# Kernel tuning notes

Hardware: AMD Instinct MI355X
Metric: run time of the kernel (lower is better)

## Reference

```python
import jax, jax.numpy as jnp
from jax import lax
import numpy as np

# ---- constants mirroring args ----
T = 8192          # signal length
NUM_CH = 64       # eeg channels
LSTM_SIZE = 256
NUM_CLS = 40
NUM_PROP = 1024   # candidate proposals before NMS
NUM_PROP_AFTER = 256
PROP_LEN = 128    # extracted window length
IOU_THRESH = 0.5


def setup_inputs() -> dict:
    key = jax.random.key(0)
    ks = jax.random.split(key, 12)
    data = jax.random.normal(ks[0], (T, NUM_CH), dtype=jnp.float32)
    # proposals: (start, end, score), 1-D temporal intervals
    starts = jax.random.uniform(ks[1], (NUM_PROP,), minval=0.0, maxval=float(T - PROP_LEN))
    lens = jax.random.uniform(ks[2], (NUM_PROP,), minval=32.0, maxval=float(PROP_LEN))
    scores = jax.random.uniform(ks[3], (NUM_PROP,))
    proposals = jnp.stack([starts, starts + lens, scores], axis=-1).astype(jnp.float32)

    H, C = LSTM_SIZE, NUM_CH
    s_ih = 1.0 / np.sqrt(C)
    s_hh = 1.0 / np.sqrt(H)
    W_ih = jax.random.uniform(ks[4], (4 * H, C), minval=-s_ih, maxval=s_ih)
    W_hh = jax.random.uniform(ks[5], (4 * H, H), minval=-s_hh, maxval=s_hh)
    b_ih = jax.random.uniform(ks[6], (4 * H,), minval=-s_hh, maxval=s_hh)
    b_hh = jax.random.uniform(ks[7], (4 * H,), minval=-s_hh, maxval=s_hh)
    s_h = 1.0 / np.sqrt(H)
    W_cls = jax.random.uniform(ks[8], (NUM_CLS, H), minval=-s_h, maxval=s_h)
    b_cls = jax.random.uniform(ks[9], (NUM_CLS,), minval=-s_h, maxval=s_h)
    W_bbox = jax.random.uniform(ks[10], (2 * NUM_CLS, H), minval=-s_h, maxval=s_h)
    b_bbox = jax.random.uniform(ks[11], (2 * NUM_CLS,), minval=-s_h, maxval=s_h)
    return {"data": data, "proposals": proposals, "W_ih": W_ih, "W_hh": W_hh,
            "b_ih": b_ih, "b_hh": b_hh, "W_cls": W_cls, "b_cls": b_cls,
            "W_bbox": W_bbox, "b_bbox": b_bbox}


def _nms_1d(starts, ends, scores, iou_thresh):
    """Greedy 1-D interval NMS. Returns indices (into original order) of the
    first NUM_PROP_AFTER surviving proposals, in descending-score order."""
    order = jnp.argsort(-scores)
    s, e = starts[order], ends[order]
    n = s.shape[0]
    idx = jnp.arange(n)

    def body(i, sup):
        inter = jnp.maximum(0.0, jnp.minimum(e[i], e) - jnp.maximum(s[i], s))
        union = (e[i] - s[i]) + (e - s) - inter
        iou = inter / jnp.maximum(union, 1e-6)
        new = sup | ((iou > iou_thresh) & (idx > i) & (~sup[i]))
        return new

    suppressed = lax.fori_loop(0, n, body, jnp.zeros(n, dtype=bool))
    keep = ~suppressed
    # stable sort: kept proposals first, preserving score order
    sel = jnp.argsort(jnp.where(keep, 0, 1), stable=True)[:NUM_PROP_AFTER]
    return order[sel]


def _lstm_last(x, W_ih, W_hh, b_ih, b_hh):
    """x: [K, L, C]; returns last hidden state [K, H] (torch gate order ifgo)."""
    K = x.shape[0]
    H = W_hh.shape[1]
    h0 = jnp.zeros((K, H), x.dtype)
    c0 = jnp.zeros((K, H), x.dtype)
    b = b_ih + b_hh

    def step(carry, xt):
        h, c = carry
        gates = xt @ W_ih.T + h @ W_hh.T + b  # [K, 4H]
        i, f, g, o = jnp.split(gates, 4, axis=-1)
        i = jax.nn.sigmoid(i)
        f = jax.nn.sigmoid(f)
        g = jnp.tanh(g)
        o = jax.nn.sigmoid(o)
        c = f * c + i * g
        h = o * jnp.tanh(c)
        return (h, c), None

    (h, _), _ = lax.scan(step, (h0, c0), jnp.swapaxes(x, 0, 1))
    return h


def reference(data, proposals, W_ih, W_hh, b_ih, b_hh, W_cls, b_cls, W_bbox, b_bbox):
    starts, ends, scores = proposals[:, 0], proposals[:, 1], proposals[:, 2]
    # NMS + truncate to num_prop_after (training branch of original)
    kept = _nms_1d(starts, ends, scores, IOU_THRESH)            # [K]
    # extract fixed-length eeg windows at proposal starts (gather)
    t0 = jnp.clip(jnp.round(starts[kept]).astype(jnp.int32), 0, T - PROP_LEN)
    win_idx = t0[:, None] + jnp.arange(PROP_LEN)[None, :]       # [K, L]
    eeg_proposals = data[win_idx]                               # [K, L, C]
    # region LSTM -> last timestep feature
    base_feat = _lstm_last(eeg_proposals, W_ih, W_hh, b_ih, b_hh)  # [K, H]
    cls_feat = base_feat @ W_cls.T + b_cls                      # [K, num_cls]
    bbox_feat = base_feat @ W_bbox.T + b_bbox                   # [K, 2*num_cls]
    return cls_feat, bbox_feat
```

## Files before the change

### kernel.cpp

```cpp
#include <hip/hip_runtime.h>
#include <math.h>

#define T_LEN 8192
#define NUM_CH 64
#define HID 256
#define NUM_CLS 40
#define NUM_PROP 1024
#define NUM_PROP_AFTER 256
#define PROP_LEN 128

#define MS 4
#define NGRP 64
#define NSL 4
#define KH 320
#define KSEGN 4
#define SEGH 80

typedef _Float16 h2_t __attribute__((ext_vector_type(2)));
union U32H2 { unsigned int u; h2_t h; };
union HU16 { _Float16 h; unsigned short u; };

#if defined(__has_builtin)
#if __has_builtin(__builtin_amdgcn_fdot2)
#define HAS_FDOT2 1
#endif
#endif

__device__ __forceinline__ float dot2f(unsigned int wa, unsigned int hb, float acc) {
    U32H2 a, b;
    a.u = wa;
    b.u = hb;
#ifdef HAS_FDOT2
    return __builtin_amdgcn_fdot2(a.h, b.h, acc, false);
#else
    return acc + (float)a.h[0] * (float)b.h[0] + (float)a.h[1] * (float)b.h[1];
#endif
}

__device__ __forceinline__ float dot8f(const uint4& w, const uint4& h, float acc) {
    acc = dot2f(w.x, h.x, acc);
    acc = dot2f(w.y, h.y, acc);
    acc = dot2f(w.z, h.z, acc);
    acc = dot2f(w.w, h.w, acc);
    return acc;
}

__device__ __forceinline__ float fsigmoid(float x) { return 1.0f / (1.0f + __expf(-x)); }
__device__ __forceinline__ float ftanh(float x) {
    float e = __expf(-2.0f * fabsf(x));
    float t = (1.0f - e) / (1.0f + e);
    return copysignf(t, x);
}

__device__ __forceinline__ unsigned int pack2(float a, float b) {
    HU16 ha, hb;
    ha.h = (_Float16)a;
    hb.h = (_Float16)b;
    return (unsigned int)ha.u | ((unsigned int)hb.u << 16);
}

__global__ __launch_bounds__(1024, 4) void fused_kernel(
    const float* __restrict__ data, const float* __restrict__ prop,
    const float* __restrict__ W_ih, const float* __restrict__ W_hh,
    const float* __restrict__ b_ih, const float* __restrict__ b_hh,
    const float* __restrict__ W_cls, const float* __restrict__ b_cls,
    const float* __restrict__ W_bbox, const float* __restrict__ b_bbox,
    float* __restrict__ out, int* __restrict__ t0s,
    unsigned int* __restrict__ Hx, unsigned int* __restrict__ cnt,
    unsigned int* __restrict__ flag) {
    __shared__ __align__(16) _Float16 hx[MS][KH];
    __shared__ __align__(16) float pp[MS][KSEGN][256];

    const int tid = threadIdx.x;
    const int g = blockIdx.x & (NGRP - 1);
    const int s = blockIdx.x >> 6;
    const int kseg = tid >> 8;
    const int rl = tid & 255;

    if (blockIdx.x == 0) {
        float* sc_p = &pp[0][0][0];
        float* ss = &pp[1][0][0];
        float* se = &pp[2][0][0];
        unsigned char* sup = (unsigned char*)&pp[3][0][0];
        unsigned long long* cmask =
            (unsigned long long*)((char*)&pp[3][0][0] + 1024);

        float ps = prop[tid * 3 + 0];
        float pe = prop[tid * 3 + 1];
        float pc = prop[tid * 3 + 2];
        sc_p[tid] = pc;
        sup[tid] = 0;
        __syncthreads();

        int r = 0;
        for (int j = 0; j < NUM_PROP; ++j) {
            float o = sc_p[j];
            r += (o > pc) || (o == pc && j < tid);
        }
        ss[r] = ps;
        se[r] = pe;
        __syncthreads();

        const float my_s = ss[tid];
        const float my_e = se[tid];
        const float my_len = my_e - my_s;
        bool mysup = false;

        for (int ci = 0; ci < 16; ++ci) {
            if (tid < 64) {
                int i = ci * 64 + tid;
                float is_ = ss[i], ie_ = se[i];
                unsigned long long m = __ballot(sup[i] != 0);
                for (int l = 0; l < 64; ++l) {
                    if (!((m >> l) & 1)) {
                        float ls = __shfl(is_, l);
                        float le = __shfl(ie_, l);
                        float inter = fmaxf(fminf(le, ie_) - fmaxf(ls, is_), 0.0f);
                        float uni = (le - ls) + (ie_ - is_) - inter;
                        float iou = inter / fmaxf(uni, 1e-6f);
                        unsigned long long nb = __ballot((tid > l) && (iou > 0.5f));
                        m |= nb;
                    }
                }
                sup[i] = (unsigned char)((m >> tid) & 1);
                if (tid == 0) cmask[ci] = ~m;
            }
            __syncthreads();
            unsigned long long am = cmask[ci];
            for (int l = 0; l < 64; ++l) {
                if ((am >> l) & 1) {
                    int i = ci * 64 + l;
                    if (tid > i && !mysup) {
                        float ls = ss[i], le = se[i];
                        float inter = fmaxf(fminf(le, my_e) - fmaxf(ls, my_s), 0.0f);
                        float uni = (le - ls) + my_len - inter;
                        if (inter / fmaxf(uni, 1e-6f) > 0.5f) mysup = true;
                    }
                }
            }
            sup[tid] = mysup ? 1 : 0;
            __syncthreads();
        }

        int myc = tid >> 6;
        unsigned long long mybit = 1ull << (tid & 63);
        int kb = 0, kt = 0;
        for (int c2 = 0; c2 < 16; ++c2) {
            int p = __popcll(cmask[c2]);
            kt += p;
            if (c2 < myc) kb += p;
        }
        kb += __popcll(cmask[myc] & (mybit - 1));
        int slot = (cmask[myc] & mybit) ? kb : (kt + (tid - kb));
        if (slot < NUM_PROP_AFTER) {
            int t0v = (int)rintf(my_s);
            t0v = max(0, min(t0v, T_LEN - PROP_LEN));
            __hip_atomic_store(&t0s[slot], t0v, __ATOMIC_RELAXED,
                               __HIP_MEMORY_SCOPE_AGENT);
        }
        asm volatile("s_waitcnt vmcnt(0)" ::: "memory");
        __syncthreads();
        if (tid == 0)
            __hip_atomic_store(flag, 1u, __ATOMIC_RELAXED,
                               __HIP_MEMORY_SCOPE_AGENT);
        __syncthreads();
    }

    uint4 Wr[10];
    {
        const int gate = rl >> 6, unit = rl & 63;
        const int grow = gate * 256 + s * 64 + unit;
        const float* __restrict__ baseh = W_hh + grow * HID;
        const float* __restrict__ basex = W_ih + grow * NUM_CH;
#pragma unroll
        for (int j = 0; j < 10; ++j) {
            const int kh = kseg * SEGH + j * 8;
            const float* src = (kh < 256) ? (baseh + kh) : (basex + (kh - 256));
            float4 f0 = *(const float4*)(src);
            float4 f1 = *(const float4*)(src + 4);
            Wr[j] = make_uint4(pack2(f0.x, f0.y), pack2(f0.z, f0.w),
                               pack2(f1.x, f1.y), pack2(f1.z, f1.w));
        }
    }

    const int aq = tid >> 6;
    const int au = tid & 63;
    float bi = 0.f, bf = 0.f, bg = 0.f, bo = 0.f, c_st = 0.f;
    if (tid < 256) {
        int u = s * 64 + au;
        bi = b_ih[u] + b_hh[u];
        bf = b_ih[256 + u] + b_hh[256 + u];
        bg = b_ih[512 + u] + b_hh[512 + u];
        bo = b_ih[768 + u] + b_hh[768 + u];
    }

    hx[tid >> 8][tid & 255] = (_Float16)0.0f;

    if (tid == 0) {
        while (__hip_atomic_load(flag, __ATOMIC_RELAXED,
                                 __HIP_MEMORY_SCOPE_AGENT) == 0u) {
            __builtin_amdgcn_s_sleep(4);
        }
    }
    __syncthreads();

    const int xs = (tid >> 6) & 3;
    const int xch = tid & 63;
    int xt0 = 0;
    if (tid >= 768) {
        xt0 = __hip_atomic_load(&t0s[g * MS + xs], __ATOMIC_RELAXED,
                                __HIP_MEMORY_SCOPE_AGENT);
        hx[xs][256 + xch] = (_Float16)data[xt0 * NUM_CH + xch];
    }

    unsigned short* HxH = (unsigned short*)Hx;
    unsigned long long* Hx64 = (unsigned long long*)Hx;
    unsigned int* cg = &cnt[g * 16];
    const int pi = tid & 15;
    __syncthreads();

    for (int t = 0; t < PROP_LEN; ++t) {
        float a0 = 0.f, a1 = 0.f, a2 = 0.f, a3 = 0.f;
#pragma unroll
        for (int j = 0; j < 10; ++j) {
            const int hb = kseg * SEGH + j * 8;
            uint4 h0 = *(const uint4*)&hx[0][hb];
            uint4 h1 = *(const uint4*)&hx[1][hb];
            uint4 h2 = *(const uint4*)&hx[2][hb];
            uint4 h3 = *(const uint4*)&hx[3][hb];
            uint4 w = Wr[j];
            a0 = dot8f(w, h0, a0);
            a1 = dot8f(w, h1, a1);
            a2 = dot8f(w, h2, a2);
            a3 = dot8f(w, h3, a3);
        }
        pp[0][kseg][rl] = a0;
        pp[1][kseg][rl] = a1;
        pp[2][kseg][rl] = a2;
        pp[3][kseg][rl] = a3;
        __syncthreads();

        const unsigned int tgt = (unsigned int)(t + 1);
        if (tid < 256) {
            float si = pp[aq][0][au] + pp[aq][1][au] + pp[aq][2][au] +
                       pp[aq][3][au] + bi;
            float sf = pp[aq][0][64 + au] + pp[aq][1][64 + au] +
                       pp[aq][2][64 + au] + pp[aq][3][64 + au] + bf;
            float sg = pp[aq][0][128 + au] + pp[aq][1][128 + au] +
                       pp[aq][2][128 + au] + pp[aq][3][128 + au] + bg;
            float so = pp[aq][0][192 + au] + pp[aq][1][192 + au] +
                       pp[aq][2][192 + au] + pp[aq][3][192 + au] + bo;
            float gi = fsigmoid(si), gf = fsigmoid(sf);
            float gg = ftanh(sg), go = fsigmoid(so);
            c_st = gf * c_st + gi * gg;
            float h = go * ftanh(c_st);
            HU16 hu;
            hu.h = (_Float16)h;
            __hip_atomic_store(
                &HxH[((((t + 1) & 1) * NGRP + g) * MS + aq) * 256 + s * 64 + au],
                hu.u, __ATOMIC_RELAXED, __HIP_MEMORY_SCOPE_AGENT);
            asm volatile("s_waitcnt vmcnt(0)" ::: "memory");
            if (au == 0)
                __hip_atomic_store(&cg[s * 4 + aq], tgt, __ATOMIC_RELAXED,
                                   __HIP_MEMORY_SCOPE_AGENT);
        } else if (tid < 512) {
            unsigned int v;
            do {
                v = __hip_atomic_load(&cg[pi], __ATOMIC_RELAXED,
                                      __HIP_MEMORY_SCOPE_AGENT);
            } while (__any(v < tgt));
            int gi2 = tid - 256;
            int sq = gi2 >> 6, w2 = gi2 & 63;
            unsigned long long hv = __hip_atomic_load(
                &Hx64[((((t + 1) & 1) * NGRP + g) * MS + sq) * 64 + w2],
                __ATOMIC_RELAXED, __HIP_MEMORY_SCOPE_AGENT);
            ((unsigned long long*)&hx[sq][0])[w2] = hv;
        } else if (tid >= 768) {
            if (t + 1 < PROP_LEN)
                hx[xs][256 + xch] = (_Float16)data[(xt0 + t + 1) * NUM_CH + xch];
        }
        __syncthreads();
    }

    if (tid < MS * 30) {
        int sq = tid / 30;
        int ml = tid % 30;
        int m = s * 30 + ml;
        const float* Wrow;
        float acc;
        int oidx;
        if (m < NUM_CLS) {
            Wrow = W_cls + m * HID;
            acc = b_cls[m];
            oidx = (g * MS + sq) * NUM_CLS + m;
        } else {
            int mb = m - NUM_CLS;
            Wrow = W_bbox + mb * HID;
            acc = b_bbox[mb];
            oidx = NUM_PROP_AFTER * NUM_CLS + (g * MS + sq) * 2 * NUM_CLS + mb;
        }
        const float4* w4 = (const float4*)Wrow;
        const _Float16* hp = &hx[sq][0];
        for (int c = 0; c < 32; ++c) {
            float4 wa = w4[c * 2 + 0];
            float4 wb = w4[c * 2 + 1];
            acc += (float)hp[c * 8 + 0] * wa.x + (float)hp[c * 8 + 1] * wa.y +
                   (float)hp[c * 8 + 2] * wa.z + (float)hp[c * 8 + 3] * wa.w +
                   (float)hp[c * 8 + 4] * wb.x + (float)hp[c * 8 + 5] * wb.y +
                   (float)hp[c * 8 + 6] * wb.z + (float)hp[c * 8 + 7] * wb.w;
        }
        out[oidx] = acc;
    }
}

extern "C" void kernel_launch(void* const* d_in, const int* in_sizes, int n_in,
                              void* d_out, int out_size, void* d_ws,
                              size_t ws_size, hipStream_t stream) {
    const float* data = (const float*)d_in[0];
    const float* prop = (const float*)d_in[1];
    const float* W_ih = (const float*)d_in[2];
    const float* W_hh = (const float*)d_in[3];
    const float* b_ih = (const float*)d_in[4];
    const float* b_hh = (const float*)d_in[5];
    const float* W_cls = (const float*)d_in[6];
    const float* b_cls = (const float*)d_in[7];
    const float* W_bbox = (const float*)d_in[8];
    const float* b_bbox = (const float*)d_in[9];
    float* out = (float*)d_out;

    int* t0s = (int*)d_ws;
    unsigned int* Hx = (unsigned int*)((char*)d_ws + 1024);
    unsigned int* cnt = (unsigned int*)((char*)d_ws + 263168);
    unsigned int* flag = (unsigned int*)((char*)d_ws + 267264);

    hipMemsetAsync((char*)d_ws + 263168, 0, 4096 + 64, stream);

    void* kargs[] = {(void*)&data,  (void*)&prop,   (void*)&W_ih,  (void*)&W_hh,
                     (void*)&b_ih,  (void*)&b_hh,   (void*)&W_cls, (void*)&b_cls,
                     (void*)&W_bbox, (void*)&b_bbox, (void*)&out,  (void*)&t0s,
                     (void*)&Hx,    (void*)&cnt,    (void*)&flag};
    hipLaunchCooperativeKernel((void*)fused_kernel, dim3(NSL * NGRP), dim3(1024),
                               kargs, 0, stream);
}
```

Measured before the change: 762.6 us.

## Replace per-slice counters with atomic group counter and per-slot t0 ready bits

Removes the global flag that every block waited on after NMS. Each proposal start is now tagged with a high ready bit, so each block polls only the slots it needs. The per-step barrier across the four slice blocks of a group becomes one fetch-add counter polled by a single thread, followed by a block barrier and a 32-bit wide copy of the hidden state by 512 threads. The x-row prefetch moves to threads 512-767 so it overlaps with the gate computation. The cost is an extra __syncthreads per timestep and contention on a single atomic counter.

```diff
diff --git a/kernel.cpp b/kernel.cpp
--- a/kernel.cpp
+++ b/kernel.cpp
@@ -65,9 +65,8 @@
     const float* __restrict__ b_ih, const float* __restrict__ b_hh,
     const float* __restrict__ W_cls, const float* __restrict__ b_cls,
     const float* __restrict__ W_bbox, const float* __restrict__ b_bbox,
-    float* __restrict__ out, int* __restrict__ t0s,
-    unsigned int* __restrict__ Hx, unsigned int* __restrict__ cnt,
-    unsigned int* __restrict__ flag) {
+    float* __restrict__ out, unsigned int* __restrict__ t0s,
+    unsigned int* __restrict__ Hx, unsigned int* __restrict__ cnt) {
     __shared__ __align__(16) _Float16 hx[MS][KH];
     __shared__ __align__(16) float pp[MS][KSEGN][256];
 
@@ -155,14 +154,10 @@
         if (slot < NUM_PROP_AFTER) {
             int t0v = (int)rintf(my_s);
             t0v = max(0, min(t0v, T_LEN - PROP_LEN));
-            __hip_atomic_store(&t0s[slot], t0v, __ATOMIC_RELAXED,
-                               __HIP_MEMORY_SCOPE_AGENT);
+            __hip_atomic_store(&t0s[slot], (unsigned int)t0v | 0x80000000u,
+                               __ATOMIC_RELAXED, __HIP_MEMORY_SCOPE_AGENT);
         }
         asm volatile("s_waitcnt vmcnt(0)" ::: "memory");
-        __syncthreads();
-        if (tid == 0)
-            __hip_atomic_store(flag, 1u, __ATOMIC_RELAXED,
-                               __HIP_MEMORY_SCOPE_AGENT);
         __syncthreads();
     }
 
@@ -196,27 +191,23 @@
 
     hx[tid >> 8][tid & 255] = (_Float16)0.0f;
 
-    if (tid == 0) {
-        while (__hip_atomic_load(flag, __ATOMIC_RELAXED,
-                                 __HIP_MEMORY_SCOPE_AGENT) == 0u) {
-            __builtin_amdgcn_s_sleep(4);
-        }
-    }
-    __syncthreads();
-
     const int xs = (tid >> 6) & 3;
     const int xch = tid & 63;
     int xt0 = 0;
-    if (tid >= 768) {
-        xt0 = __hip_atomic_load(&t0s[g * MS + xs], __ATOMIC_RELAXED,
-                                __HIP_MEMORY_SCOPE_AGENT);
+    if (tid >= 512 && tid < 768) {
+        const unsigned int* tp = &t0s[g * MS + xs];
+        unsigned int tv;
+        for (;;) {
+            tv = __hip_atomic_load(tp, __ATOMIC_RELAXED, __HIP_MEMORY_SCOPE_AGENT);
+            if (tv & 0x80000000u) break;
+            __builtin_amdgcn_s_sleep(8);
+        }
+        xt0 = (int)(tv & 0x7FFFFFFFu);
         hx[xs][256 + xch] = (_Float16)data[xt0 * NUM_CH + xch];
     }
 
     unsigned short* HxH = (unsigned short*)Hx;
-    unsigned long long* Hx64 = (unsigned long long*)Hx;
     unsigned int* cg = &cnt[g * 16];
-    const int pi = tid & 15;
     __syncthreads();
 
     for (int t = 0; t < PROP_LEN; ++t) {
@@ -240,7 +231,6 @@
         pp[3][kseg][rl] = a3;
         __syncthreads();
 
-        const unsigned int tgt = (unsigned int)(t + 1);
         if (tid < 256) {
             float si = pp[aq][0][au] + pp[aq][1][au] + pp[aq][2][au] +
                        pp[aq][3][au] + bi;
@@ -261,23 +251,26 @@
                 hu.u, __ATOMIC_RELAXED, __HIP_MEMORY_SCOPE_AGENT);
             asm volatile("s_waitcnt vmcnt(0)" ::: "memory");
             if (au == 0)
-                __hip_atomic_store(&cg[s * 4 + aq], tgt, __ATOMIC_RELAXED,
-                                   __HIP_MEMORY_SCOPE_AGENT);
-        } else if (tid < 512) {
-            unsigned int v;
-            do {
-                v = __hip_atomic_load(&cg[pi], __ATOMIC_RELAXED,
-                                      __HIP_MEMORY_SCOPE_AGENT);
-            } while (__any(v < tgt));
-            int gi2 = tid - 256;
-            int sq = gi2 >> 6, w2 = gi2 & 63;
-            unsigned long long hv = __hip_atomic_load(
-                &Hx64[((((t + 1) & 1) * NGRP + g) * MS + sq) * 64 + w2],
+                __hip_atomic_fetch_add(cg, 1u, __ATOMIC_RELAXED,
+                                       __HIP_MEMORY_SCOPE_AGENT);
+        } else if (tid < 768 && t + 1 < PROP_LEN) {
+            hx[xs][256 + xch] = (_Float16)data[(xt0 + t + 1) * NUM_CH + xch];
+        }
+
+        const unsigned int tgt = 16u * (unsigned int)(t + 1);
+        if (tid == 0) {
+            while (__hip_atomic_load(cg, __ATOMIC_RELAXED,
+                                     __HIP_MEMORY_SCOPE_AGENT) < tgt) {
+                __builtin_amdgcn_s_sleep(1);
+            }
+        }
+        __syncthreads();
+        if (tid < 512) {
+            int sq = tid >> 7, w = tid & 127;
+            unsigned int v = __hip_atomic_load(
+                &Hx[((((t + 1) & 1) * NGRP + g) * MS + sq) * 128 + w],
                 __ATOMIC_RELAXED, __HIP_MEMORY_SCOPE_AGENT);
-            ((unsigned long long*)&hx[sq][0])[w2] = hv;
-        } else if (tid >= 768) {
-            if (t + 1 < PROP_LEN)
-                hx[xs][256 + xch] = (_Float16)data[(xt0 + t + 1) * NUM_CH + xch];
+            ((unsigned int*)hx)[sq * 160 + w] = v;
         }
         __syncthreads();
     }
@@ -328,17 +321,16 @@
     const float* b_bbox = (const float*)d_in[9];
     float* out = (float*)d_out;
 
-    int* t0s = (int*)d_ws;
-    unsigned int* Hx = (unsigned int*)((char*)d_ws + 1024);
-    unsigned int* cnt = (unsigned int*)((char*)d_ws + 263168);
-    unsigned int* flag = (unsigned int*)((char*)d_ws + 267264);
-
-    hipMemsetAsync((char*)d_ws + 263168, 0, 4096 + 64, stream);
+    unsigned int* t0s = (unsigned int*)d_ws;
+    unsigned int* cnt = (unsigned int*)((char*)d_ws + 1024);
+    unsigned int* Hx = (unsigned int*)((char*)d_ws + 5120);
+
+    hipMemsetAsync(d_ws, 0, 5120, stream);
 
     void* kargs[] = {(void*)&data,  (void*)&prop,   (void*)&W_ih,  (void*)&W_hh,
                      (void*)&b_ih,  (void*)&b_hh,   (void*)&W_cls, (void*)&b_cls,
                      (void*)&W_bbox, (void*)&b_bbox, (void*)&out,  (void*)&t0s,
-                     (void*)&Hx,    (void*)&cnt,    (void*)&flag};
+                     (void*)&Hx,    (void*)&cnt};
     hipLaunchCooperativeKernel((void*)fused_kernel, dim3(NSL * NGRP), dim3(1024),
                                kargs, 0, stream);
 }
```

Result: faster. 746.3 us (-2.1%).
